# Kernel tuning notes

Measured on AMD Instinct MI355X. Metric: run time of the kernel, lower is better.

The kernel has to match this reference:

```python
import jax, jax.numpy as jnp
import numpy as np

IN_SIZE = 1024
HID = 1024


def setup_inputs() -> dict:
    key = jax.random.key(0)
    ks = jax.random.split(key, 5)
    B, T = 32, 512
    bound = 1.0 / np.sqrt(HID)
    x = jax.random.normal(ks[0], (B, T, IN_SIZE), dtype=jnp.float32)
    h0 = jnp.zeros((B, HID), dtype=jnp.float32)
    c0 = jnp.zeros((B, HID), dtype=jnp.float32)
    W_ih = jax.random.uniform(ks[1], (4 * HID, IN_SIZE), minval=-bound, maxval=bound, dtype=jnp.float32)
    W_hh = jax.random.uniform(ks[2], (4 * HID, HID), minval=-bound, maxval=bound, dtype=jnp.float32)
    b_ih = jax.random.uniform(ks[3], (4 * HID,), minval=-bound, maxval=bound, dtype=jnp.float32)
    b_hh = jax.random.uniform(ks[4], (4 * HID,), minval=-bound, maxval=bound, dtype=jnp.float32)
    return {"x": x, "h0": h0, "c0": c0, "W_ih": W_ih, "W_hh": W_hh, "b_ih": b_ih, "b_hh": b_hh}


def _lstm_final_h(x, h0, c0, W_ih, W_hh, b_ih, b_hh):
    # Precompute input projections for all timesteps: [B,T,4H]
    xg = jnp.einsum('bti,gi->btg', x, W_ih) + b_ih + b_hh
    H = h0.shape[-1]

    def step(carry, xg_t):
        h, c = carry
        gates = xg_t + h @ W_hh.T  # [B,4H]
        i, f, g, o = jnp.split(gates, 4, axis=-1)  # torch LSTMCell gate order
        i = jax.nn.sigmoid(i)
        f = jax.nn.sigmoid(f)
        g = jnp.tanh(g)
        o = jax.nn.sigmoid(o)
        c_new = f * c + i * g
        h_new = o * jnp.tanh(c_new)
        return (h_new, c_new), None

    (h_final, _), _ = jax.lax.scan(step, (h0, c0), jnp.swapaxes(xg, 0, 1))
    return h_final


def reference(x, h0, c0, W_ih, W_hh, b_ih, b_hh):
    return _lstm_final_h(x, h0, c0, W_ih, W_hh, b_ih, b_hh)
```

## Files before the change

kernel.cpp:

```cpp
#include <hip/hip_runtime.h>
#include <stdint.h>

typedef __attribute__((ext_vector_type(8))) short short8;
typedef __attribute__((ext_vector_type(4))) float f32x4;

__device__ __forceinline__ unsigned short f32_to_bf16(float f) {
    unsigned int u = __float_as_uint(f);
    unsigned int r = (u + 0x7FFF + ((u >> 16) & 1)) >> 16;
    return (unsigned short)r;
}
__device__ __forceinline__ float bf16_to_f32(unsigned short s) {
    return __uint_as_float(((unsigned int)s) << 16);
}

__device__ __forceinline__ float sigm_fast(float z) {
    return __fdividef(1.f, 1.f + __expf(-z));
}
__device__ __forceinline__ float tanh_fast(float z) {
    float a = fabsf(z);
    float e = __expf(-2.f * a);
    float r = __fdividef(1.f - e, 1.f + e);
    return copysignf(r, z);
}

__global__ void cvt_bf16_kernel(const float* __restrict__ in,
                                unsigned short* __restrict__ out, int n) {
    int i = (blockIdx.x * blockDim.x + threadIdx.x) * 4;
    if (i >= n) return;
    float4 v = *(const float4*)(in + i);
    ushort4 o;
    o.x = f32_to_bf16(v.x);
    o.y = f32_to_bf16(v.y);
    o.z = f32_to_bf16(v.z);
    o.w = f32_to_bf16(v.w);
    *(ushort4*)(out + i) = o;
}

__global__ void bias_add_kernel(const float* __restrict__ bi,
                                const float* __restrict__ bh,
                                float* __restrict__ bias) {
    int i = blockIdx.x * blockDim.x + threadIdx.x;
    bias[i] = bi[i] + bh[i];
}

__global__ void fill_kernel(unsigned int* __restrict__ p, unsigned int v, int n) {
    int i = blockIdx.x * blockDim.x + threadIdx.x;
    if (i < n) p[i] = v;
}

__global__ void hG_init_kernel(const float* __restrict__ h0,
                               unsigned int* __restrict__ hG) {
    int D = blockIdx.x * blockDim.x + threadIdx.x;
    int i2 = D & 3, b = (D >> 2) & 31, kq = D >> 7;
    int j = kq * 8 + i2 * 2;
    unsigned int lo = f32_to_bf16(h0[b * 1024 + j]);
    unsigned int hi = f32_to_bf16(h0[b * 1024 + j + 1]);
    hG[D] = lo | (hi << 16);
}

#define LDP 40

__global__ __launch_bounds__(256) void gemm_xproj(
    const unsigned short* __restrict__ A,
    const unsigned short* __restrict__ B,
    const float* __restrict__ bias,
    unsigned short* __restrict__ C) {
    __shared__ unsigned short As[64][LDP];
    __shared__ unsigned short Bs[64][LDP];
    const int tid  = threadIdx.x;
    const int lane = tid & 63;
    const int wave = tid >> 6;
    const int m0 = blockIdx.y * 64;
    const int n0 = blockIdx.x * 64;
    const int wm = (wave & 1) * 32;
    const int wn = (wave >> 1) * 32;

    f32x4 acc[2][2] = {};

    const int sr = tid >> 2;
    const int sk = (tid & 3) * 8;
    const int fr = lane & 15;
    const int fk = (lane >> 4) * 8;

    for (int k0 = 0; k0 < 1024; k0 += 32) {
        uint4 av = *(const uint4*)&A[(m0 + sr) * 1024 + k0 + sk];
        uint4 bv = *(const uint4*)&B[(n0 + sr) * 1024 + k0 + sk];
        __syncthreads();
        *(uint4*)&As[sr][sk] = av;
        *(uint4*)&Bs[sr][sk] = bv;
        __syncthreads();
        short8 a0 = *(const short8*)&As[wm + fr][fk];
        short8 a1 = *(const short8*)&As[wm + 16 + fr][fk];
        short8 b0 = *(const short8*)&Bs[wn + fr][fk];
        short8 b1 = *(const short8*)&Bs[wn + 16 + fr][fk];
        acc[0][0] = __builtin_amdgcn_mfma_f32_16x16x32_bf16(a0, b0, acc[0][0], 0, 0, 0);
        acc[0][1] = __builtin_amdgcn_mfma_f32_16x16x32_bf16(a0, b1, acc[0][1], 0, 0, 0);
        acc[1][0] = __builtin_amdgcn_mfma_f32_16x16x32_bf16(a1, b0, acc[1][0], 0, 0, 0);
        acc[1][1] = __builtin_amdgcn_mfma_f32_16x16x32_bf16(a1, b1, acc[1][1], 0, 0, 0);
    }

    const int col = lane & 15;
    const int rq  = (lane >> 4) * 4;
    for (int mt = 0; mt < 2; mt++) {
        for (int nt = 0; nt < 2; nt++) {
            int gcol = n0 + wn + nt * 16 + col;
            float bv = bias[gcol];
            for (int r = 0; r < 4; r++) {
                int grow = m0 + wm + mt * 16 + rq + r;
                C[(size_t)grow * 4096 + gcol] = f32_to_bf16(acc[mt][nt][r] + bv);
            }
        }
    }
}

__global__ __launch_bounds__(512, 1) void lstm_persist(
    const float* __restrict__ Whh,
    const unsigned short* __restrict__ xg,
    const float* __restrict__ c0,
    unsigned int* __restrict__ hSeq,
    float* __restrict__ out) {
    __shared__ float partial[4][4][32][16];
    __shared__ unsigned short hout[32][16];

    const int tid  = threadIdx.x;
    const int bid  = blockIdx.x;
    const int j0   = bid * 16;
    const int lane = tid & 63;
    const int wave = tid >> 6;
    const int ks   = wave >> 1;
    const int nt   = wave & 1;
    const int col  = lane & 15;
    const int quad = lane >> 4;

    short8 af[4][8];
#pragma unroll
    for (int mt = 0; mt < 4; ++mt) {
#pragma unroll
        for (int u = 0; u < 8; ++u) {
            const float* wr = Whh + (size_t)(mt * 1024 + j0 + col) * 1024
                              + (ks * 8 + u) * 32 + quad * 8;
            float4 wa = *(const float4*)wr;
            float4 wb = *(const float4*)(wr + 4);
            short8 v;
            v[0] = (short)f32_to_bf16(wa.x); v[1] = (short)f32_to_bf16(wa.y);
            v[2] = (short)f32_to_bf16(wa.z); v[3] = (short)f32_to_bf16(wa.w);
            v[4] = (short)f32_to_bf16(wb.x); v[5] = (short)f32_to_bf16(wb.y);
            v[6] = (short)f32_to_bf16(wb.z); v[7] = (short)f32_to_bf16(wb.w);
            af[mt][u] = v;
        }
        asm volatile("" ::: "memory");
    }

    const int eb = tid >> 4;
    const int ej = tid & 15;
    float cst = c0[eb * 1024 + j0 + ej];

    const int kq0  = bid * 2;
    const int bofs = nt * 16 + col;

    __syncthreads();

    for (int t = 0; t < 512; ++t) {
        const unsigned int* hR = hSeq + (size_t)t * 16384;
        unsigned int*       hW = hSeq + (size_t)(t + 1) * 16384;

        const unsigned short* px = xg + (size_t)(eb * 512 + t) * 4096 + j0 + ej;
        unsigned short x0 = px[0];
        unsigned short x1 = px[1024];
        unsigned short x2 = px[2048];
        unsigned short x3 = px[3072];

        uint4 bv[8];
        for (;;) {
#pragma unroll
            for (int u = 0; u < 8; ++u) {
                int kc = ks * 8 + u;
                const unsigned int* p = hR + ((kc * 4 + quad) * 32 + bofs) * 4;
                asm volatile("global_load_dwordx4 %0, %1, off sc1"
                             : "=v"(bv[u]) : "v"(p) : "memory");
            }
            asm volatile("s_waitcnt vmcnt(0)" ::: "memory");
            __builtin_amdgcn_sched_barrier(0);
            bool ok = true;
#pragma unroll
            for (int u = 0; u < 8; ++u)
                ok = ok && (bv[u].x != 0xFFFFFFFFu) && (bv[u].y != 0xFFFFFFFFu) &&
                           (bv[u].z != 0xFFFFFFFFu) && (bv[u].w != 0xFFFFFFFFu);
            if (__all(ok)) break;
            __builtin_amdgcn_s_sleep(1);
        }

        f32x4 acc[4] = {};
#pragma unroll
        for (int u = 0; u < 8; ++u) {
            union { uint4 u4; short8 s8; } cv;
            cv.u4 = bv[u];
#pragma unroll
            for (int mt = 0; mt < 4; ++mt)
                acc[mt] = __builtin_amdgcn_mfma_f32_16x16x32_bf16(af[mt][u], cv.s8,
                                                                  acc[mt], 0, 0, 0);
        }
#pragma unroll
        for (int mt = 0; mt < 4; ++mt)
            *(f32x4*)&partial[ks][mt][bofs][quad * 4] = acc[mt];
        __syncthreads();

        float z[4];
#pragma unroll
        for (int q = 0; q < 4; ++q)
            z[q] = partial[0][q][eb][ej] + partial[1][q][eb][ej] +
                   partial[2][q][eb][ej] + partial[3][q][eb][ej];
        z[0] += bf16_to_f32(x0);
        z[1] += bf16_to_f32(x1);
        z[2] += bf16_to_f32(x2);
        z[3] += bf16_to_f32(x3);
        float ig = sigm_fast(z[0]);
        float fg = sigm_fast(z[1]);
        float gg = tanh_fast(z[2]);
        float og = sigm_fast(z[3]);
        cst = fg * cst + ig * gg;
        float hn = og * tanh_fast(cst);
        hout[eb][ej] = f32_to_bf16(hn);
        if (t == 511) {
            out[eb * 1024 + j0 + ej] = hn;
            break;
        }
        __syncthreads();

        if (tid < 64) {
            int bb = tid & 31, kl = tid >> 5;
            uint2 d0 = *(const uint2*)&hout[bb][kl * 8];
            uint2 d1 = *(const uint2*)&hout[bb][kl * 8 + 4];
            unsigned int* p = hW + ((kq0 + kl) * 32 + bb) * 4;
            asm volatile("global_store_dwordx2 %0, %1, off sc1"
                         :: "v"(p), "v"(d0) : "memory");
            asm volatile("global_store_dwordx2 %0, %1, off sc1\n\ts_waitcnt vmcnt(0)"
                         :: "v"(p + 2), "v"(d1) : "memory");
        }
    }
}

extern "C" void kernel_launch(void* const* d_in, const int* in_sizes, int n_in,
                              void* d_out, int out_size, void* d_ws, size_t ws_size,
                              hipStream_t stream) {
    const float* x    = (const float*)d_in[0];
    const float* h0   = (const float*)d_in[1];
    const float* c0   = (const float*)d_in[2];
    const float* Wih  = (const float*)d_in[3];
    const float* Whh  = (const float*)d_in[4];
    const float* b_ih = (const float*)d_in[5];
    const float* b_hh = (const float*)d_in[6];
    float* out = (float*)d_out;
    char* ws = (char*)d_ws;

    unsigned short* xg   = (unsigned short*)(ws);
    unsigned short* xA   = (unsigned short*)(ws + 134217728);
    unsigned short* wB   = (unsigned short*)(ws + 167772160);
    float*          bias = (float*)(ws + 176160768);
    unsigned int*   hSeq = (unsigned int*)(ws + 134217728);

    cvt_bf16_kernel<<<16384, 256, 0, stream>>>(x, xA, 16777216);
    cvt_bf16_kernel<<<4096, 256, 0, stream>>>(Wih, wB, 4194304);
    bias_add_kernel<<<16, 256, 0, stream>>>(b_ih, b_hh, bias);

    dim3 g1(64, 256);
    gemm_xproj<<<g1, 256, 0, stream>>>(xA, wB, bias, xg);

    fill_kernel<<<32704, 256, 0, stream>>>(hSeq + 16384, 0xFFFFFFFFu, 511 * 16384);
    hG_init_kernel<<<64, 256, 0, stream>>>(h0, hSeq);

    lstm_persist<<<64, 512, 0, stream>>>(Whh, xg, c0, hSeq, out);
}
```

Before: 2.052 ms.

## Double-buffer partial sums and publish h directly via lane shuffles

The partial-sum shared buffer is double-buffered by timestep parity, and padded, so the second __syncthreads per step can be removed. Each thread now packs its bf16 h value with its neighbour's through a shuffle and stores it straight to the global h sequence, replacing the LDS staging plus 64-thread dwordx2 store path. This shortens the per-step critical path of the persistent recurrent loop. In exchange, many more threads issue small dword stores with a wait after each, and correctness now depends on the parity buffering being enough to avoid write-after-read races on the partial sums.

```diff
diff --git a/kernel.cpp b/kernel.cpp
--- a/kernel.cpp
+++ b/kernel.cpp
@@ -119,8 +119,7 @@
     const float* __restrict__ c0,
     unsigned int* __restrict__ hSeq,
     float* __restrict__ out) {
-    __shared__ float partial[4][4][32][16];
-    __shared__ unsigned short hout[32][16];
+    __shared__ float partial[2][4][4][32][20];
 
     const int tid  = threadIdx.x;
     const int bid  = blockIdx.x;
@@ -157,12 +156,12 @@
 
     const int kq0  = bid * 2;
     const int bofs = nt * 16 + col;
+    const int poff = ((kq0 + (ej >> 3)) * 32 + eb) * 4 + ((ej & 7) >> 1);
 
     __syncthreads();
 
     for (int t = 0; t < 512; ++t) {
-        const unsigned int* hR = hSeq + (size_t)t * 16384;
-        unsigned int*       hW = hSeq + (size_t)(t + 1) * 16384;
+        const unsigned int* hR = hSeq + ((size_t)t << 14);
 
         const unsigned short* px = xg + (size_t)(eb * 512 + t) * 4096 + j0 + ej;
         unsigned short x0 = px[0];
@@ -200,16 +199,17 @@
                 acc[mt] = __builtin_amdgcn_mfma_f32_16x16x32_bf16(af[mt][u], cv.s8,
                                                                   acc[mt], 0, 0, 0);
         }
+        const int p = t & 1;
 #pragma unroll
         for (int mt = 0; mt < 4; ++mt)
-            *(f32x4*)&partial[ks][mt][bofs][quad * 4] = acc[mt];
+            *(f32x4*)&partial[p][ks][mt][bofs][quad * 4] = acc[mt];
         __syncthreads();
 
         float z[4];
 #pragma unroll
         for (int q = 0; q < 4; ++q)
-            z[q] = partial[0][q][eb][ej] + partial[1][q][eb][ej] +
-                   partial[2][q][eb][ej] + partial[3][q][eb][ej];
+            z[q] = partial[p][0][q][eb][ej] + partial[p][1][q][eb][ej] +
+                   partial[p][2][q][eb][ej] + partial[p][3][q][eb][ej];
         z[0] += bf16_to_f32(x0);
         z[1] += bf16_to_f32(x1);
         z[2] += bf16_to_f32(x2);
@@ -220,22 +220,18 @@
         float og = sigm_fast(z[3]);
         cst = fg * cst + ig * gg;
         float hn = og * tanh_fast(cst);
-        hout[eb][ej] = f32_to_bf16(hn);
         if (t == 511) {
             out[eb * 1024 + j0 + ej] = hn;
             break;
         }
-        __syncthreads();
-
-        if (tid < 64) {
-            int bb = tid & 31, kl = tid >> 5;
-            uint2 d0 = *(const uint2*)&hout[bb][kl * 8];
-            uint2 d1 = *(const uint2*)&hout[bb][kl * 8 + 4];
-            unsigned int* p = hW + ((kq0 + kl) * 32 + bb) * 4;
-            asm volatile("global_store_dwordx2 %0, %1, off sc1"
-                         :: "v"(p), "v"(d0) : "memory");
-            asm volatile("global_store_dwordx2 %0, %1, off sc1\n\ts_waitcnt vmcnt(0)"
-                         :: "v"(p + 2), "v"(d1) : "memory");
+
+        float hp = __shfl_xor(hn, 1);
+        unsigned lo16 = f32_to_bf16(hn), hi16 = f32_to_bf16(hp);
+        unsigned pack = lo16 | (hi16 << 16);
+        unsigned int* pw = hSeq + ((size_t)(t + 1) << 14) + poff;
+        if ((ej & 1) == 0) {
+            asm volatile("global_store_dword %0, %1, off sc1\n\ts_waitcnt vmcnt(0)"
+                         :: "v"(pw), "v"(pack) : "memory");
         }
     }
 }
```

Result: faster. 1.924 ms (-6.3%).
